# Kernel tuning notes

Hardware: AMD Instinct MI355X
Metric: run time of the kernel (lower is better)

The kernel has to match this reference:

```python
import jax, jax.numpy as jnp
import numpy as np

GRID_MIN, GRID_MAX, GRID_SIZE = -4.0, 4.0, 12
BANDWIDTH = (GRID_MAX - GRID_MIN) / max(GRID_SIZE - 1, 1)  # 8/11


def setup_inputs() -> dict:
    key = jax.random.key(0)
    k1, k2, k3, k4 = jax.random.split(key, 4)
    B, I, O, G = 16384, 512, 512, GRID_SIZE
    x = jax.random.normal(k1, (B, I), dtype=jnp.float32)
    coeff = jax.random.normal(k2, (I, O, G), dtype=jnp.float32) * 0.05
    base_w = jax.random.normal(k3, (O, I), dtype=jnp.float32) * (1.0 / np.sqrt(I))
    base_b = jax.random.normal(k4, (O,), dtype=jnp.float32) * 0.01
    centers = jnp.linspace(GRID_MIN, GRID_MAX, G, dtype=jnp.float32)
    return {"x": x, "coeff": coeff, "base_w": base_w, "base_b": base_b, "centers": centers}


def reference(x, coeff, base_w, base_b, centers):
    # RBF basis: [B, I, G]
    diff = (x[..., None] - centers) / jnp.float32(BANDWIDTH)
    basis = jnp.exp(-0.5 * diff * diff)
    # spline contraction over in_dim and grid: [B, O]
    spline = jnp.einsum('big,iog->bo', basis, coeff)
    # residual base linear (torch Linear: x @ W^T + b)
    return spline + x @ base_w.T + base_b
```

## Files before the change

### kernel.cpp

```cpp
#include <hip/hip_runtime.h>
#include <hip/hip_bf16.h>


#define M_DIM 16384
#define N_DIM 512
#define I_DIM 512
#define KTOT  6656
#define NSTEP 104

typedef short short8 __attribute__((ext_vector_type(8)));
typedef float f32x16 __attribute__((ext_vector_type(16)));
typedef unsigned int u32x4 __attribute__((ext_vector_type(4)));

#define CVTPK(dst, lo, hi) \
  asm("v_cvt_pk_bf16_f32 %0, %1, %2" : "=v"(dst) : "v"(lo), "v"(hi))

__device__ __forceinline__ unsigned short f2bf(float f) {
  union { float f; unsigned int u; } c; c.f = f;
  unsigned int r = (c.u + 0x7FFFu + ((c.u >> 16) & 1)) >> 16;
  return (unsigned short)r;
}

__global__ __launch_bounds__(256) void prep_w(const float* __restrict__ coeff,
                                              const float* __restrict__ base_w,
                                              unsigned short* __restrict__ Wb) {
  int t = blockIdx.x * 256 + threadIdx.x;
  int o = t / 1664;
  int k4 = (t - o * 1664) * 4;
  int ic = k4 / 832;
  int rem = k4 - ic * 832;
  int slot = rem >> 6;
  int ii = rem & 63;
  int i = ic * 64 + ii;
  float v0, v1, v2, v3;
  if (slot == 0) {
    const float4 bw = *(const float4*)(base_w + (size_t)o * I_DIM + i);
    v0 = bw.x; v1 = bw.y; v2 = bw.z; v3 = bw.w;
  } else {
    int g = slot - 1;
    const float* cp = coeff + (size_t)i * (N_DIM * 12) + o * 12 + g;
    v0 = cp[0]; v1 = cp[6144]; v2 = cp[2 * 6144]; v3 = cp[3 * 6144];
  }
  ushort4 s;
  s.x = f2bf(v0); s.y = f2bf(v1); s.z = f2bf(v2); s.w = f2bf(v3);
  *(ushort4*)(Wb + (size_t)o * KTOT + k4) = s;
}

__global__ __launch_bounds__(512, 2) void kan_gemm(const float* __restrict__ x,
                                                   const unsigned short* __restrict__ Wb,
                                                   const float* __restrict__ bias,
                                                   float* __restrict__ out) {
  __shared__ unsigned short Asw[2][128 * 64];
  __shared__ unsigned short Bsw[2][256 * 64];

  const int tid  = threadIdx.x;
  const int lane = tid & 63;
  const int wid  = tid >> 6;
  const int wm   = wid >> 2, wn = wid & 3;

  const int rb = blockIdx.x >> 1;
  const int cb = blockIdx.x & 1;
  const int M0 = rb * 128;
  const int N0 = cb * 256;

  const int sr  = tid >> 2;
  const int skq = tid & 3;
  const float* xg = x + (size_t)(M0 + sr) * I_DIM + skq * 16;
  const int aswz  = (sr & 7) << 4;
  const int aoff0 = sr * 128 + ((skq * 32) ^ aswz);
  const int aoff1 = sr * 128 + ((skq * 32 + 16) ^ aswz);

  const int cg = lane >> 3;
  const int uu = lane & 7;
  const unsigned short* bsrc[4];
  int bdstoff[4];
#pragma unroll
  for (int q = 0; q < 4; ++q) {
    int c0 = wid * 32 + q * 8;
    bsrc[q] = Wb + (size_t)(N0 + c0 + cg) * KTOT + ((uu ^ cg) << 3);
    bdstoff[q] = c0 * 64;
  }

  const int l31  = lane & 31;
  const int rswz = (lane & 7) << 4;
  const int kc   = (lane >> 5) * 16;
  const int aro0 = (wm * 64 + l31) * 128;
  const int aro1 = aro0 + 32 * 128;
  const int bro0 = (wn * 64 + l31) * 128;
  const int bro1 = bro0 + 32 * 128;

  f32x16 acc[2][2];
#pragma unroll
  for (int i = 0; i < 2; ++i)
#pragma unroll
    for (int j = 0; j < 2; ++j)
#pragma unroll
      for (int r = 0; r < 16; ++r) acc[i][j][r] = 0.f;

  float4 xq[4];
#pragma unroll
  for (int q = 0; q < 4; ++q) xq[q] = *(const float4*)(xg + q * 4);
  float bb[16], ff[16];
  int gslot = 0, gic = 0;

  auto emitA = [&](char* pA) {
    unsigned int w[8];
    if (gslot == 0) {
      float f[16];
#pragma unroll
      for (int q = 0; q < 4; ++q) {
        f[q*4+0] = xq[q].x; f[q*4+1] = xq[q].y; f[q*4+2] = xq[q].z; f[q*4+3] = xq[q].w;
      }
#pragma unroll
      for (int j = 0; j < 8; ++j) CVTPK(w[j], f[2*j], f[2*j+1]);
      *(u32x4*)(pA + aoff0) = (u32x4){w[0], w[1], w[2], w[3]};
      *(u32x4*)(pA + aoff1) = (u32x4){w[4], w[5], w[6], w[7]};
#pragma unroll
      for (int j = 0; j < 16; ++j) {
        float u = fmaf(f[j], 1.375f, 5.5f);
        bb[j] = exp2f(-0.72134752044448170f * u * u);
        ff[j] = exp2f(fmaf(u, 1.44269504088896340f, -0.72134752044448170f));
      }
      if (gic < 7) {
        const float* xn = xg + (gic + 1) * 64;
#pragma unroll
        for (int q = 0; q < 4; ++q) xq[q] = *(const float4*)(xn + q * 4);
        ++gic;
      }
    } else {
#pragma unroll
      for (int j = 0; j < 8; ++j) CVTPK(w[j], bb[2*j], bb[2*j+1]);
      *(u32x4*)(pA + aoff0) = (u32x4){w[0], w[1], w[2], w[3]};
      *(u32x4*)(pA + aoff1) = (u32x4){w[4], w[5], w[6], w[7]};
#pragma unroll
      for (int j = 0; j < 16; ++j) {
        bb[j] *= ff[j];
        ff[j] *= 0.36787944117144233f;
      }
    }
    gslot = (gslot == 12) ? 0 : gslot + 1;
  };

  emitA((char*)&Asw[0][0]);
#pragma unroll
  for (int q = 0; q < 4; ++q)
    __builtin_amdgcn_global_load_lds(
        (const __attribute__((address_space(1))) void*)(bsrc[q]),
        (__attribute__((address_space(3))) void*)(&Bsw[0][bdstoff[q]]), 16, 0, 0);
  __syncthreads();

  int buf = 0;
  for (int ks = 0; ks < NSTEP; ++ks) {
    const int nxt = buf ^ 1;
    if (ks < NSTEP - 1) {
      const size_t ko = (size_t)(ks + 1) * 64;
#pragma unroll
      for (int q = 0; q < 4; ++q)
        __builtin_amdgcn_global_load_lds(
            (const __attribute__((address_space(1))) void*)(bsrc[q] + ko),
            (__attribute__((address_space(3))) void*)(&Bsw[nxt][bdstoff[q]]), 16, 0, 0);
      emitA((char*)&Asw[nxt][0]);
    }
    const char* pA = (const char*)&Asw[buf][0];
    const char* pB = (const char*)&Bsw[buf][0];
#pragma unroll
    for (int s = 0; s < 4; ++s) {
      const int cbyte = (s * 32 + kc) ^ rswz;
      short8 a0 = *(const short8*)(pA + aro0 + cbyte);
      short8 a1 = *(const short8*)(pA + aro1 + cbyte);
      short8 b0 = *(const short8*)(pB + bro0 + cbyte);
      short8 b1 = *(const short8*)(pB + bro1 + cbyte);
      acc[0][0] = __builtin_amdgcn_mfma_f32_32x32x16_bf16(a0, b0, acc[0][0], 0, 0, 0);
      acc[0][1] = __builtin_amdgcn_mfma_f32_32x32x16_bf16(a0, b1, acc[0][1], 0, 0, 0);
      acc[1][0] = __builtin_amdgcn_mfma_f32_32x32x16_bf16(a1, b0, acc[1][0], 0, 0, 0);
      acc[1][1] = __builtin_amdgcn_mfma_f32_32x32x16_bf16(a1, b1, acc[1][1], 0, 0, 0);
    }
    __syncthreads();
    buf = nxt;
  }

  float bv[2];
#pragma unroll
  for (int fn = 0; fn < 2; ++fn) bv[fn] = bias[N0 + wn * 64 + fn * 32 + l31];
  const int rbase = (lane >> 5) * 4;
#pragma unroll
  for (int fm = 0; fm < 2; ++fm) {
#pragma unroll
    for (int fn = 0; fn < 2; ++fn) {
      const size_t cix = (size_t)(N0 + wn * 64 + fn * 32 + l31);
#pragma unroll
      for (int r = 0; r < 16; ++r) {
        int row = M0 + wm * 64 + fm * 32 + (r & 3) + 8 * (r >> 2) + rbase;
        out[(size_t)row * N_DIM + cix] = acc[fm][fn][r] + bv[fn];
      }
    }
  }
}

extern "C" void kernel_launch(void* const* d_in, const int* in_sizes, int n_in,
                              void* d_out, int out_size, void* d_ws, size_t ws_size,
                              hipStream_t stream) {
  const float* x      = (const float*)d_in[0];
  const float* coeff  = (const float*)d_in[1];
  const float* base_w = (const float*)d_in[2];
  const float* base_b = (const float*)d_in[3];
  unsigned short* Wb = (unsigned short*)d_ws;

  prep_w<<<3328, 256, 0, stream>>>(coeff, base_w, Wb);
  kan_gemm<<<256, 512, 0, stream>>>(x, Wb, base_b, (float*)d_out);
}
```

Before: 144.2 us.

## Reorder weight workspace and LDS tiles into k-group-major 8-element chunks

The prep kernel now writes bf16 weights as [k-group of 8][output][8], and the GEMM stages both A and B tiles in LDS as [k-group][row][8] instead of row-major with an XOR swizzle. Each wave's global-to-LDS loads become contiguous 16-byte lanes, and each MFMA fragment read becomes a simple linear offset with no swizzle arithmetic. This may cause LDS bank conflicts, since 32 lanes read rows 16 bytes apart while the other half-wave sits in a distant k-group. The prep kernel's writes are also scattered differently.

```diff
diff --git a/kernel.cpp b/kernel.cpp
--- a/kernel.cpp
+++ b/kernel.cpp
@@ -23,10 +23,13 @@
 
 __global__ __launch_bounds__(256) void prep_w(const float* __restrict__ coeff,
                                               const float* __restrict__ base_w,
-                                              unsigned short* __restrict__ Wb) {
+                                              unsigned short* __restrict__ Wb2) {
   int t = blockIdx.x * 256 + threadIdx.x;
-  int o = t / 1664;
-  int k4 = (t - o * 1664) * 4;
+  int e0 = (t & 1) * 4;
+  int go = t >> 1;
+  int o  = go & 511;
+  int g  = go >> 9;
+  int k4 = g * 8 + e0;
   int ic = k4 / 832;
   int rem = k4 - ic * 832;
   int slot = rem >> 6;
@@ -37,21 +40,21 @@
     const float4 bw = *(const float4*)(base_w + (size_t)o * I_DIM + i);
     v0 = bw.x; v1 = bw.y; v2 = bw.z; v3 = bw.w;
   } else {
-    int g = slot - 1;
-    const float* cp = coeff + (size_t)i * (N_DIM * 12) + o * 12 + g;
+    int gg = slot - 1;
+    const float* cp = coeff + (size_t)i * (N_DIM * 12) + o * 12 + gg;
     v0 = cp[0]; v1 = cp[6144]; v2 = cp[2 * 6144]; v3 = cp[3 * 6144];
   }
   ushort4 s;
   s.x = f2bf(v0); s.y = f2bf(v1); s.z = f2bf(v2); s.w = f2bf(v3);
-  *(ushort4*)(Wb + (size_t)o * KTOT + k4) = s;
+  *(ushort4*)(Wb2 + (size_t)go * 8 + e0) = s;
 }
 
 __global__ __launch_bounds__(512, 2) void kan_gemm(const float* __restrict__ x,
-                                                   const unsigned short* __restrict__ Wb,
+                                                   const unsigned short* __restrict__ Wb2,
                                                    const float* __restrict__ bias,
                                                    float* __restrict__ out) {
-  __shared__ unsigned short Asw[2][128 * 64];
-  __shared__ unsigned short Bsw[2][256 * 64];
+  __shared__ unsigned short Asw[2][8 * 128 * 8];
+  __shared__ unsigned short Bsw[2][8 * 256 * 8];
 
   const int tid  = threadIdx.x;
   const int lane = tid & 63;
@@ -63,31 +66,23 @@
   const int M0 = rb * 128;
   const int N0 = cb * 256;
 
-  const int sr  = tid >> 2;
-  const int skq = tid & 3;
-  const float* xg = x + (size_t)(M0 + sr) * I_DIM + skq * 16;
-  const int aswz  = (sr & 7) << 4;
-  const int aoff0 = sr * 128 + ((skq * 32) ^ aswz);
-  const int aoff1 = sr * 128 + ((skq * 32 + 16) ^ aswz);
-
-  const int cg = lane >> 3;
-  const int uu = lane & 7;
+  const int arow = tid & 127;
+  const int kgp  = tid >> 7;
+  const float* xg = x + (size_t)(M0 + arow) * I_DIM + kgp * 16;
+  const int aoff0 = ((kgp * 2) * 128 + arow) * 16;
+  const int aoff1 = ((kgp * 2 + 1) * 128 + arow) * 16;
+
   const unsigned short* bsrc[4];
-  int bdstoff[4];
+  int bdst[4];
 #pragma unroll
   for (int q = 0; q < 4; ++q) {
-    int c0 = wid * 32 + q * 8;
-    bsrc[q] = Wb + (size_t)(N0 + c0 + cg) * KTOT + ((uu ^ cg) << 3);
-    bdstoff[q] = c0 * 64;
-  }
-
-  const int l31  = lane & 31;
-  const int rswz = (lane & 7) << 4;
-  const int kc   = (lane >> 5) * 16;
-  const int aro0 = (wm * 64 + l31) * 128;
-  const int aro1 = aro0 + 32 * 128;
-  const int bro0 = (wn * 64 + l31) * 128;
-  const int bro1 = bro0 + 32 * 128;
+    bsrc[q] = Wb2 + ((size_t)wid * 512 + N0 + q * 64 + lane) * 8;
+    bdst[q] = (wid * 256 + q * 64) * 16;
+  }
+
+  const int l31 = lane & 31;
+  const int aBase = ((lane >> 5) * 128 + wm * 64 + l31) * 16;
+  const int bBase = ((lane >> 5) * 256 + wn * 64 + l31) * 16;
 
   f32x16 acc[2][2];
 #pragma unroll
@@ -146,30 +141,31 @@
   for (int q = 0; q < 4; ++q)
     __builtin_amdgcn_global_load_lds(
         (const __attribute__((address_space(1))) void*)(bsrc[q]),
-        (__attribute__((address_space(3))) void*)(&Bsw[0][bdstoff[q]]), 16, 0, 0);
+        (__attribute__((address_space(3))) void*)((char*)&Bsw[0][0] + bdst[q]), 16, 0, 0);
   __syncthreads();
 
   int buf = 0;
   for (int ks = 0; ks < NSTEP; ++ks) {
     const int nxt = buf ^ 1;
     if (ks < NSTEP - 1) {
-      const size_t ko = (size_t)(ks + 1) * 64;
+      const size_t ko = (size_t)(ks + 1) * 32768;
 #pragma unroll
       for (int q = 0; q < 4; ++q)
         __builtin_amdgcn_global_load_lds(
             (const __attribute__((address_space(1))) void*)(bsrc[q] + ko),
-            (__attribute__((address_space(3))) void*)(&Bsw[nxt][bdstoff[q]]), 16, 0, 0);
+            (__attribute__((address_space(3))) void*)((char*)&Bsw[nxt][0] + bdst[q]), 16, 0, 0);
       emitA((char*)&Asw[nxt][0]);
     }
     const char* pA = (const char*)&Asw[buf][0];
     const char* pB = (const char*)&Bsw[buf][0];
 #pragma unroll
     for (int s = 0; s < 4; ++s) {
-      const int cbyte = (s * 32 + kc) ^ rswz;
-      short8 a0 = *(const short8*)(pA + aro0 + cbyte);
-      short8 a1 = *(const short8*)(pA + aro1 + cbyte);
-      short8 b0 = *(const short8*)(pB + bro0 + cbyte);
-      short8 b1 = *(const short8*)(pB + bro1 + cbyte);
+      const char* a = pA + aBase + s * 4096;
+      const char* b = pB + bBase + s * 8192;
+      short8 a0 = *(const short8*)(a);
+      short8 a1 = *(const short8*)(a + 512);
+      short8 b0 = *(const short8*)(b);
+      short8 b1 = *(const short8*)(b + 512);
       acc[0][0] = __builtin_amdgcn_mfma_f32_32x32x16_bf16(a0, b0, acc[0][0], 0, 0, 0);
       acc[0][1] = __builtin_amdgcn_mfma_f32_32x32x16_bf16(a0, b1, acc[0][1], 0, 0, 0);
       acc[1][0] = __builtin_amdgcn_mfma_f32_32x32x16_bf16(a1, b0, acc[1][0], 0, 0, 0);
@@ -204,8 +200,8 @@
   const float* coeff  = (const float*)d_in[1];
   const float* base_w = (const float*)d_in[2];
   const float* base_b = (const float*)d_in[3];
-  unsigned short* Wb = (unsigned short*)d_ws;
-
-  prep_w<<<3328, 256, 0, stream>>>(coeff, base_w, Wb);
-  kan_gemm<<<256, 512, 0, stream>>>(x, Wb, base_b, (float*)d_out);
-}
+  unsigned short* Wb2 = (unsigned short*)d_ws;
+
+  prep_w<<<3328, 256, 0, stream>>>(coeff, base_w, Wb2);
+  kan_gemm<<<256, 512, 0, stream>>>(x, Wb2, base_b, (float*)d_out);
+}
```

Result: faster. 138.0 us (-4.3%).
